# Kernel optimization log

Measured on AMD Instinct MI355X. Metric: run time of the kernel, lower is better.

## Reference

```python
import jax, jax.numpy as jnp
import numpy as np

V, E, H, L = 10000, 256, 512, 2
B, T, S = 64, 64, 128
NEG = -1e6


def setup_inputs() -> dict:
    key = jax.random.key(0)
    ks = jax.random.split(key, 20)
    sc = 0.02
    inp = {
        "x": jax.random.randint(ks[0], (B, T), 0, V),
        "enc_outputs": jax.random.normal(ks[1], (B, S, H), jnp.float32),
        "h0": jax.random.normal(ks[2], (L, B, H), jnp.float32),
        "valid_lens": jax.random.randint(ks[3], (B,), 1, S + 1).astype(jnp.int32),
        # params
        "emb": jax.random.normal(ks[4], (V, E), jnp.float32) * sc,
        "Wq": jax.random.normal(ks[5], (H, H), jnp.float32) * sc,
        "Wk": jax.random.normal(ks[6], (H, H), jnp.float32) * sc,
        "wv": jax.random.normal(ks[7], (H,), jnp.float32) * sc,
        "W_ih0": jax.random.normal(ks[8], (3 * H, H + E), jnp.float32) * sc,
        "W_hh0": jax.random.normal(ks[9], (3 * H, H), jnp.float32) * sc,
        "b_ih0": jnp.zeros((3 * H,), jnp.float32),
        "b_hh0": jnp.zeros((3 * H,), jnp.float32),
        "W_ih1": jax.random.normal(ks[10], (3 * H, H), jnp.float32) * sc,
        "W_hh1": jax.random.normal(ks[11], (3 * H, H), jnp.float32) * sc,
        "b_ih1": jnp.zeros((3 * H,), jnp.float32),
        "b_hh1": jnp.zeros((3 * H,), jnp.float32),
        "Wd": jax.random.normal(ks[12], (V, H), jnp.float32) * sc,
        "bd": jnp.zeros((V,), jnp.float32),
    }
    return inp


def _gru_cell(x, h, W_ih, W_hh, b_ih, b_hh):
    # PyTorch GRU cell math
    gi = x @ W_ih.T + b_ih  # (B, 3H)
    gh = h @ W_hh.T + b_hh
    ir, iz, in_ = jnp.split(gi, 3, axis=-1)
    hr, hz, hn = jnp.split(gh, 3, axis=-1)
    r = jax.nn.sigmoid(ir + hr)
    z = jax.nn.sigmoid(iz + hz)
    n = jnp.tanh(in_ + r * hn)
    return (1.0 - z) * n + z * h


def reference(x, enc_outputs, h0, valid_lens, emb, Wq, Wk, wv,
              W_ih0, W_hh0, b_ih0, b_hh0, W_ih1, W_hh1, b_ih1, b_hh1, Wd, bd):
    X = emb[x]                     # (B, T, E)
    Xt = jnp.transpose(X, (1, 0, 2))  # (T, B, E) time-major
    k_proj = jnp.einsum('bsh,oh->bso', enc_outputs, Wk)  # precompute W_k(keys)
    mask = jnp.arange(S)[None, :] < valid_lens[:, None]  # (B, S)

    def step(h, x_t):
        q = h[-1]                                      # (B, H) last-layer hidden
        q_proj = q @ Wq.T                              # (B, H)
        feats = jnp.tanh(q_proj[:, None, :] + k_proj)  # (B, S, H)
        scores = jnp.einsum('bsh,h->bs', feats, wv)
        scores = jnp.where(mask, scores, NEG)
        attn = jax.nn.softmax(scores, axis=-1)
        context = jnp.einsum('bs,bsh->bh', attn, enc_outputs)
        inp = jnp.concatenate([context, x_t], axis=-1)  # (B, H+E)
        h0n = _gru_cell(inp, h[0], W_ih0, W_hh0, b_ih0, b_hh0)
        h1n = _gru_cell(h0n, h[1], W_ih1, W_hh1, b_ih1, b_hh1)
        hn = jnp.stack([h0n, h1n])
        return hn, h1n

    _, ys = jax.lax.scan(step, h0, Xt)       # ys: (T, B, H)
    logits = jnp.einsum('tbh,vh->tbv', ys, Wd) + bd
    return jnp.transpose(logits, (1, 0, 2))  # (B, T, V)
```

## Files before the change

kernel.cpp:

```cpp
#include <hip/hip_runtime.h>
#include <hip/hip_bf16.h>

#define Bd 64
#define Td 64
#define Sd 128
#define Hd 512
#define Ed 256
#define Vd 10000
#define NBLK 256

#define W0IH 0
#define W0HH 4608
#define W1IH 7680
#define W1HH 10752
#define WTOT 13824

typedef __attribute__((ext_vector_type(8))) short bf16x8;
typedef __attribute__((ext_vector_type(4))) float f32x4;

__device__ __forceinline__ float fast_tanh(float x) {
  float e = __expf(-2.0f * fabsf(x));
  float r = (1.0f - e) / (1.0f + e);
  return copysignf(r, x);
}
__device__ __forceinline__ float fast_sigmoid(float x) {
  return 1.0f / (1.0f + __expf(-x));
}
__device__ __forceinline__ float bf2f(unsigned short u) {
  return __uint_as_float(((unsigned int)u) << 16);
}
__device__ __forceinline__ void st_llc(float* p, float v) {
  __hip_atomic_store(p, v, __ATOMIC_RELAXED, __HIP_MEMORY_SCOPE_AGENT);
}
__device__ __forceinline__ int q4(int k, int b) {
  return (k >> 2) * 256 + b * 4 + (k & 3);
}

__device__ __forceinline__ void gbar(int* arrive, int* go, int ep, int blk, int tid) {
  __syncthreads();
  if (tid == 0)
    __hip_atomic_store(&arrive[blk], ep, __ATOMIC_RELAXED, __HIP_MEMORY_SCOPE_AGENT);
  if (blk == 0) {
    if (tid < 64) {
      for (;;) {
        int a0 = __hip_atomic_load(&arrive[tid], __ATOMIC_RELAXED,
                                   __HIP_MEMORY_SCOPE_AGENT);
        int a1 = __hip_atomic_load(&arrive[tid + 64], __ATOMIC_RELAXED,
                                   __HIP_MEMORY_SCOPE_AGENT);
        int a2 = __hip_atomic_load(&arrive[tid + 128], __ATOMIC_RELAXED,
                                   __HIP_MEMORY_SCOPE_AGENT);
        int a3 = __hip_atomic_load(&arrive[tid + 192], __ATOMIC_RELAXED,
                                   __HIP_MEMORY_SCOPE_AGENT);
        if (a0 >= ep && a1 >= ep && a2 >= ep && a3 >= ep) break;
        __builtin_amdgcn_s_sleep(2);
      }
    }
    __syncthreads();
    if (tid == 0)
      __hip_atomic_store(go, ep, __ATOMIC_RELAXED, __HIP_MEMORY_SCOPE_AGENT);
  }
  if (tid == 0) {
    while (__hip_atomic_load(go, __ATOMIC_RELAXED, __HIP_MEMORY_SCOPE_AGENT) < ep) {
      __builtin_amdgcn_s_sleep(1);
    }
    __builtin_amdgcn_fence(__ATOMIC_ACQUIRE, "agent");
  }
  __syncthreads();
}

__global__ void k_gemm_kp(const float* __restrict__ A, const float* __restrict__ W,
                          unsigned short* __restrict__ C, int M, int N, int K) {
  __shared__ __align__(16) float As[16][64];
  __shared__ __align__(16) float Ws[16][64];
  int m0 = blockIdx.x * 64, n0 = blockIdx.y * 64;
  int tid = threadIdx.x;
  int tx = tid & 15, ty = tid >> 4;
  float acc[4][4] = {};
  for (int k0 = 0; k0 < K; k0 += 16) {
#pragma unroll
    for (int i = 0; i < 4; i++) {
      int e = tid + i * 256;
      int r = e >> 4, c = e & 15;
      As[c][r] = A[(long)(m0 + r) * K + k0 + c];
      Ws[c][r] = W[(long)(n0 + r) * K + k0 + c];
    }
    __syncthreads();
#pragma unroll
    for (int k = 0; k < 16; k++) {
      float a_[4], w_[4];
#pragma unroll
      for (int i = 0; i < 4; i++) a_[i] = As[k][ty * 4 + i];
#pragma unroll
      for (int j = 0; j < 4; j++) w_[j] = Ws[k][tx * 4 + j];
#pragma unroll
      for (int i = 0; i < 4; i++)
#pragma unroll
        for (int j = 0; j < 4; j++) acc[i][j] += a_[i] * w_[j];
    }
    __syncthreads();
  }
#pragma unroll
  for (int i = 0; i < 4; i++)
#pragma unroll
    for (int j = 0; j < 4; j++) {
      __hip_bfloat16 h = __float2bfloat16(acc[i][j]);
      C[(long)(m0 + ty * 4 + i) * N + n0 + tx * 4 + j] = *(unsigned short*)&h;
    }
}

__global__ __launch_bounds__(256) void k_logits(
    const unsigned short* __restrict__ ysbf, const unsigned short* __restrict__ Wdbf,
    const float* __restrict__ bd, float* __restrict__ out, int N) {
  int m0 = blockIdx.x * 64, n0 = blockIdx.y * 64;
  int w = threadIdx.x >> 6, lane = threadIdx.x & 63;
  int row = lane & 15, kg = lane >> 4;
  int mw = m0 + w * 16;
  f32x4 acc[4] = {};
  const unsigned short* Arow = ysbf + (size_t)(mw + row) * 512 + kg * 8;
  for (int k0 = 0; k0 < 512; k0 += 32) {
    bf16x8 af = *(const bf16x8*)(Arow + k0);
#pragma unroll
    for (int nn = 0; nn < 4; nn++) {
      int ncol = n0 + nn * 16 + row;
      bf16x8 bfv = {};
      if (ncol < N) bfv = *(const bf16x8*)(Wdbf + (size_t)ncol * 512 + k0 + kg * 8);
      acc[nn] = __builtin_amdgcn_mfma_f32_16x16x32_bf16(af, bfv, acc[nn], 0, 0, 0);
    }
  }
#pragma unroll
  for (int nn = 0; nn < 4; nn++) {
    int ncol = n0 + nn * 16 + row;
    if (ncol < N) {
      float bv = bd[ncol];
#pragma unroll
      for (int r = 0; r < 4; r++) {
        int mm = mw + kg * 4 + r;
        int t_ = mm >> 6, b_ = mm & 63;
        out[((size_t)(b_ * Td + t_)) * N + ncol] = acc[nn][r] + bv;
      }
    }
  }
}

__global__ void k_tobf(const float* __restrict__ src, unsigned short* __restrict__ dst,
                       long n) {
  long i = (long)blockIdx.x * 1024 + threadIdx.x;
  if (i < n) {
    __hip_bfloat16 h = __float2bfloat16(src[i]);
    dst[i] = *(unsigned short*)&h;
  }
}

__global__ void k_embT(const int* __restrict__ x, const float* __restrict__ emb,
                       float* __restrict__ embTf) {
  __shared__ int rows[64];
  int t = blockIdx.x;
  if (threadIdx.x < 64) rows[threadIdx.x] = x[threadIdx.x * Td + t];
  __syncthreads();
  int e = threadIdx.x;
  for (int b = 0; b < 64; b++) {
    embTf[(size_t)t * 16384 + q4(e, b)] = emb[(long)rows[b] * Ed + e];
  }
}

template <bool C0>
__device__ __forceinline__ void cell_phase(
    int blk, int tid, int t, const float* __restrict__ aT,
    const float* __restrict__ embTf, const float* __restrict__ hT,
    const float* wIH, const float* wHH, const float* __restrict__ bih,
    const float* __restrict__ bhh, const float* __restrict__ den,
    float* __restrict__ houtT, unsigned short* __restrict__ ysbf, float* scratch) {
  int lane = tid & 63;
  int w = tid >> 6;
  const int RIH = C0 ? 768 : 512;
  float* ps = scratch;
  float* psE = scratch + 3072;
  if (w < 8) {
    int strm = w >> 2, qk = w & 3;
    const float* A = (strm == 0 ? aT : hT) + qk * 32 * 256;
    float a[6] = {0.f, 0.f, 0.f, 0.f, 0.f, 0.f};
#pragma unroll 8
    for (int k4 = 0; k4 < 32; k4++) {
      float4 av = *(const float4*)&A[k4 * 256 + lane * 4];
#pragma unroll
      for (int r = 0; r < 6; r++) {
        const float* wr = (strm == 0 ? wIH + (size_t)r * RIH : wHH + (size_t)r * 512) +
                          qk * 128 + k4 * 4;
        float4 w4 = *(const float4*)wr;
        a[r] += av.x * w4.x + av.y * w4.y + av.z * w4.z + av.w * w4.w;
      }
    }
    int base = strm * 6;
#pragma unroll
    for (int r = 0; r < 6; r++) ps[((base + r) * 4 + qk) * 64 + lane] = a[r];
  } else if (C0 && w < 12) {
    int qe = w - 8;
    const float* ef = embTf + (size_t)t * 16384 + qe * 16 * 256;
    float a[6] = {0.f, 0.f, 0.f, 0.f, 0.f, 0.f};
#pragma unroll 8
    for (int k4 = 0; k4 < 16; k4++) {
      float4 ev = *(const float4*)&ef[k4 * 256 + lane * 4];
#pragma unroll
      for (int r = 0; r < 6; r++) {
        const float* wr = wIH + (size_t)r * 768 + 512 + qe * 64 + k4 * 4;
        float4 w4 = *(const float4*)wr;
        a[r] += ev.x * w4.x + ev.y * w4.y + ev.z * w4.z + ev.w * w4.w;
      }
    }
#pragma unroll
    for (int r = 0; r < 6; r++) psE[(r * 4 + qe) * 64 + lane] = a[r];
  }
  __syncthreads();
  if (tid < 128) {
    int jl = tid >> 6, b = tid & 63;
    float invd = C0 ? (1.0f / den[b]) : 1.0f;
#define RD(R)                                                              \
  (ps[((R)*4 + 0) * 64 + b] + ps[((R)*4 + 1) * 64 + b] +                   \
   ps[((R)*4 + 2) * 64 + b] + ps[((R)*4 + 3) * 64 + b])
#define RE(R)                                                              \
  (psE[((R)*4 + 0) * 64 + b] + psE[((R)*4 + 1) * 64 + b] +                 \
   psE[((R)*4 + 2) * 64 + b] + psE[((R)*4 + 3) * 64 + b])
    float ir = RD(0 + jl);
    float iz = RD(2 + jl);
    float in = RD(4 + jl);
    if (C0) {
      ir = ir * invd + RE(0 + jl);
      iz = iz * invd + RE(2 + jl);
      in = in * invd + RE(4 + jl);
    }
    float hr = RD(6 + jl);
    float hz = RD(8 + jl);
    float hn_ = RD(10 + jl);
#undef RD
#undef RE
    int j = blk * 2 + jl;
    float r = fast_sigmoid(ir + hr + bih[j] + bhh[j]);
    float z = fast_sigmoid(iz + hz + bih[Hd + j] + bhh[Hd + j]);
    float n = fast_tanh(in + bih[2 * Hd + j] + r * (hn_ + bhh[2 * Hd + j]));
    float hp = hT[q4(j, b)];
    float out = (1.f - z) * n + z * hp;
    st_llc(&houtT[q4(j, b)], out);
    if (!C0) {
      __hip_bfloat16 hb = __float2bfloat16(out);
      ysbf[((size_t)t * 64 + b) * 512 + j] = *(unsigned short*)&hb;
    }
  }
}

__global__ __launch_bounds__(1024, 1) void k_decoder(
    const float* __restrict__ h0_in, const int* __restrict__ vlen,
    const float* __restrict__ Wq, const float* __restrict__ wvp,
    const float* __restrict__ Wih0, const float* __restrict__ Whh0,
    const float* __restrict__ bih0, const float* __restrict__ bhh0,
    const float* __restrict__ Wih1, const float* __restrict__ Whh1,
    const float* __restrict__ bih1, const float* __restrict__ bhh1,
    const unsigned short* __restrict__ kpbf, const unsigned short* __restrict__ encbf,
    const float* __restrict__ embTf, int* bar, float* qpN, float* ctxT,
    float* den, float* h0TA, float* h0TB, float* h1TA, float* h1TB,
    unsigned short* ysbf) {
  __shared__ __align__(16) float wLDS[WTOT];
  __shared__ __align__(16) float WqL[1024];
  __shared__ __align__(16) unsigned short kpL[32 * 512];
  __shared__ __align__(16) unsigned short encL[32 * 512];
  __shared__ __align__(16) float scratch[4608];
  int blk = blockIdx.x, tid = threadIdx.x;
  int lane = tid & 63;
  int w = tid >> 6;
  int battn = blk >> 2, q = blk & 3;
  int* arrive = bar;
  int* go = bar + NBLK;
  int ep = 0;

  {
    int j0 = blk * 2;
#pragma unroll
    for (int rr = 0; rr < 6; rr++) {
      int g = rr >> 1, jl = rr & 1;
      int row = g * Hd + j0 + jl;
      const float* s0 = Wih0 + (size_t)row * 768;
      for (int k = tid; k < 768; k += 1024) wLDS[W0IH + rr * 768 + k] = s0[k];
      const float* s1 = Whh0 + (size_t)row * Hd;
      for (int k = tid; k < Hd; k += 1024) wLDS[W0HH + rr * 512 + k] = s1[k];
      const float* s2 = Wih1 + (size_t)row * Hd;
      for (int k = tid; k < Hd; k += 1024) wLDS[W1IH + rr * 512 + k] = s2[k];
      const float* s3 = Whh1 + (size_t)row * Hd;
      for (int k = tid; k < Hd; k += 1024) wLDS[W1HH + rr * 512 + k] = s3[k];
    }
    WqL[tid] = Wq[(size_t)(blk * 2 + (tid >> 9)) * Hd + (tid & 511)];
    const uint4* ksrc = (const uint4*)(kpbf + ((size_t)battn * Sd + q * 32) * Hd);
    const uint4* esrc = (const uint4*)(encbf + ((size_t)battn * Sd + q * 32) * Hd);
    uint4* kdst = (uint4*)kpL;
    uint4* edst = (uint4*)encL;
    for (int i = tid; i < 2048; i += 1024) {
      kdst[i] = ksrc[i];
      edst[i] = esrc[i];
    }
  }
  float wvr[8];
#pragma unroll
  for (int i = 0; i < 8; i++) wvr[i] = wvp[lane * 8 + i];

  if (blk < Bd) {
    int b = blk;
    for (int k = tid; k < Hd; k += 1024) {
      st_llc(&h0TA[q4(k, b)], h0_in[(0 * Bd + b) * Hd + k]);
      st_llc(&h1TA[q4(k, b)], h0_in[(1 * Bd + b) * Hd + k]);
    }
  }
  if (tid < 128) st_llc(&ctxT[blk * 128 + tid], 0.f);
  if (blk < Bd && tid == 128) st_llc(&den[blk], 0.f);
  gbar(arrive, go, ++ep, blk, tid);

  for (int t = 0; t < Td; t++) {
    const float* h0prev = (t & 1) ? h0TB : h0TA;
    float* h0next = (t & 1) ? h0TA : h0TB;
    const float* h1prev = (t & 1) ? h1TB : h1TA;
    float* h1next = (t & 1) ? h1TA : h1TB;

    {
      int rl = w >> 3, ks = w & 7;
      const float* qrow = &WqL[rl * 512 + ks * 64];
      const float* hp4 = h1prev + (ks * 16) * 256 + lane * 4;
      float acc = 0.f;
#pragma unroll
      for (int kk = 0; kk < 64; kk += 4) {
        float4 hv = *(const float4*)&hp4[(kk >> 2) * 256];
        acc += hv.x * qrow[kk] + hv.y * qrow[kk + 1] + hv.z * qrow[kk + 2] +
               hv.w * qrow[kk + 3];
      }
      scratch[w * 64 + lane] = acc;
      __syncthreads();
      if (tid < 128) {
        int rl2 = tid >> 6, b = tid & 63;
        float s = 0.f;
#pragma unroll
        for (int qq = 0; qq < 8; qq++) s += scratch[(rl2 * 8 + qq) * 64 + b];
        st_llc(&qpN[(size_t)b * 512 + blk * 2 + rl2], s);
      }
    }
    gbar(arrive, go, ++ep, blk, tid);

    {
      int b = battn;
      float* sc = scratch;
      float qv[8];
      const float* qb = qpN + (size_t)b * 512 + lane * 8;
#pragma unroll
      for (int i = 0; i < 8; i++) qv[i] = qb[i];
      int vl = vlen[b];
#pragma unroll
      for (int si = 0; si < 2; si++) {
        int sl = w * 2 + si;
        uint4 kw = *(const uint4*)&kpL[sl * 512 + lane * 8];
        float f0 = __uint_as_float(kw.x << 16);
        float f1 = __uint_as_float(kw.x & 0xffff0000u);
        float f2 = __uint_as_float(kw.y << 16);
        float f3 = __uint_as_float(kw.y & 0xffff0000u);
        float f4 = __uint_as_float(kw.z << 16);
        float f5 = __uint_as_float(kw.z & 0xffff0000u);
        float f6 = __uint_as_float(kw.w << 16);
        float f7 = __uint_as_float(kw.w & 0xffff0000u);
        float acc = wvr[0] * fast_tanh(qv[0] + f0) + wvr[1] * fast_tanh(qv[1] + f1) +
                    wvr[2] * fast_tanh(qv[2] + f2) + wvr[3] * fast_tanh(qv[3] + f3) +
                    wvr[4] * fast_tanh(qv[4] + f4) + wvr[5] * fast_tanh(qv[5] + f5) +
                    wvr[6] * fast_tanh(qv[6] + f6) + wvr[7] * fast_tanh(qv[7] + f7);
#pragma unroll
        for (int off = 1; off < 64; off <<= 1) acc += __shfl_xor(acc, off);
        if (lane == 0) {
          int s = q * 32 + sl;
          sc[sl] = (s < vl) ? __expf(acc) : 0.f;
        }
      }
      __syncthreads();
      if (tid < 32) {
        float p2 = sc[tid];
#pragma unroll
        for (int off = 1; off < 32; off <<= 1) p2 += __shfl_xor(p2, off, 32);
        if (tid == 0) atomicAdd(&den[b], p2);
      }
      if (tid < 512) {
        float acc = 0.f;
#pragma unroll 8
        for (int s = 0; s < 32; s++) acc += sc[s] * bf2f(encL[s * 512 + tid]);
        atomicAdd(&ctxT[q4(tid, b)], acc);
      }
    }
    gbar(arrive, go, ++ep, blk, tid);

    cell_phase<true>(blk, tid, t, ctxT, embTf, h0prev, wLDS + W0IH, wLDS + W0HH,
                     bih0, bhh0, den, h0next, nullptr, scratch);
    gbar(arrive, go, ++ep, blk, tid);

    if (tid < 128) st_llc(&ctxT[blk * 128 + tid], 0.f);
    if (blk < Bd && tid == 128) st_llc(&den[blk], 0.f);
    cell_phase<false>(blk, tid, t, h0next, nullptr, h1prev, wLDS + W1IH,
                      wLDS + W1HH, bih1, bhh1, nullptr, h1next, ysbf, scratch);
    gbar(arrive, go, ++ep, blk, tid);
  }
}

extern "C" void kernel_launch(void* const* d_in, const int* in_sizes, int n_in,
                              void* d_out, int out_size, void* d_ws, size_t ws_size,
                              hipStream_t stream) {
  const int* x = (const int*)d_in[0];
  const float* enc = (const float*)d_in[1];
  const float* h0 = (const float*)d_in[2];
  const int* vlen = (const int*)d_in[3];
  const float* emb = (const float*)d_in[4];
  const float* Wq = (const float*)d_in[5];
  const float* Wk = (const float*)d_in[6];
  const float* wv = (const float*)d_in[7];
  const float* W_ih0 = (const float*)d_in[8];
  const float* W_hh0 = (const float*)d_in[9];
  const float* b_ih0 = (const float*)d_in[10];
  const float* b_hh0 = (const float*)d_in[11];
  const float* W_ih1 = (const float*)d_in[12];
  const float* W_hh1 = (const float*)d_in[13];
  const float* b_ih1 = (const float*)d_in[14];
  const float* b_hh1 = (const float*)d_in[15];
  const float* Wd = (const float*)d_in[16];
  const float* bd = (const float*)d_in[17];
  float* out = (float*)d_out;

  char* p = (char*)d_ws;
  int* bar = (int*)p;
  p += 2048;
  unsigned short* kpbf = (unsigned short*)p;
  p += (size_t)Bd * Sd * Hd * 2;
  unsigned short* encbf = (unsigned short*)p;
  p += (size_t)Bd * Sd * Hd * 2;
  unsigned short* Wdbf = (unsigned short*)p;
  p += (size_t)Vd * Hd * 2;
  unsigned short* ysbf = (unsigned short*)p;
  p += (size_t)Td * Bd * Hd * 2;
  float* embTf = (float*)p;
  p += (size_t)Td * Ed * Bd * 4;
  float* qpN = (float*)p;   p += (size_t)Bd * Hd * 4;
  float* ctxT = (float*)p;  p += (size_t)Hd * Bd * 4;
  float* den = (float*)p;   p += 256;
  float* h0TA = (float*)p;  p += (size_t)Hd * Bd * 4;
  float* h0TB = (float*)p;  p += (size_t)Hd * Bd * 4;
  float* h1TA = (float*)p;  p += (size_t)Hd * Bd * 4;
  float* h1TB = (float*)p;

  hipMemsetAsync(bar, 0, 2048, stream);

  k_gemm_kp<<<dim3(128, 8), 256, 0, stream>>>(enc, Wk, kpbf, Bd * Sd, Hd, Hd);
  long nenc = (long)Bd * Sd * Hd;
  k_tobf<<<(nenc + 1023) / 1024, 1024, 0, stream>>>(enc, encbf, nenc);
  long nwd = (long)Vd * Hd;
  k_tobf<<<(nwd + 1023) / 1024, 1024, 0, stream>>>(Wd, Wdbf, nwd);
  k_embT<<<Td, 256, 0, stream>>>(x, emb, embTf);
  k_decoder<<<NBLK, 1024, 0, stream>>>(h0, vlen, Wq, wv, W_ih0, W_hh0, b_ih0,
                                       b_hh0, W_ih1, W_hh1, b_ih1, b_hh1, kpbf,
                                       encbf, embTf, bar, qpN, ctxT, den, h0TA,
                                       h0TB, h1TA, h1TB, ysbf);
  k_logits<<<dim3(64, 157), 256, 0, stream>>>(ysbf, Wdbf, bd, out, Vd);
}
```

Before: 3.762 ms.

## Precompute embedding input-gate projections for all timesteps outside the recurrent loop

```diff
diff --git a/kernel.cpp b/kernel.cpp
--- a/kernel.cpp
+++ b/kernel.cpp
@@ -108,6 +108,47 @@
     }
 }
 
+__global__ void k_embG(const int* __restrict__ x, const float* __restrict__ emb,
+                       const float* __restrict__ Wih0, float* __restrict__ embG) {
+  __shared__ __align__(16) float As[16][64];
+  __shared__ __align__(16) float Bs[16][64];
+  __shared__ int xs[64];
+  int m0 = blockIdx.x * 64, t = blockIdx.y;
+  int tid = threadIdx.x;
+  int tx = tid & 15, ty = tid >> 4;
+  if (tid < 64) xs[tid] = x[tid * Td + t];
+  __syncthreads();
+  float acc[4][4] = {};
+  for (int k0 = 0; k0 < Ed; k0 += 16) {
+#pragma unroll
+    for (int i = 0; i < 4; i++) {
+      int e = tid + i * 256;
+      int r = e >> 4, c = e & 15;
+      As[c][r] = Wih0[(size_t)(m0 + r) * 768 + 512 + k0 + c];
+      Bs[c][r] = emb[(size_t)xs[r] * Ed + k0 + c];
+    }
+    __syncthreads();
+#pragma unroll
+    for (int k = 0; k < 16; k++) {
+      float a_[4], b_[4];
+#pragma unroll
+      for (int i = 0; i < 4; i++) a_[i] = As[k][ty * 4 + i];
+#pragma unroll
+      for (int j = 0; j < 4; j++) b_[j] = Bs[k][tx * 4 + j];
+#pragma unroll
+      for (int i = 0; i < 4; i++)
+#pragma unroll
+        for (int j = 0; j < 4; j++) acc[i][j] += a_[i] * b_[j];
+    }
+    __syncthreads();
+  }
+#pragma unroll
+  for (int i = 0; i < 4; i++)
+#pragma unroll
+    for (int j = 0; j < 4; j++)
+      embG[(size_t)(m0 + ty * 4 + i) * 4096 + t * 64 + tx * 4 + j] = acc[i][j];
+}
+
 __global__ __launch_bounds__(256) void k_logits(
     const unsigned short* __restrict__ ysbf, const unsigned short* __restrict__ Wdbf,
     const float* __restrict__ bd, float* __restrict__ out, int N) {
@@ -151,22 +192,10 @@
   }
 }
 
-__global__ void k_embT(const int* __restrict__ x, const float* __restrict__ emb,
-                       float* __restrict__ embTf) {
-  __shared__ int rows[64];
-  int t = blockIdx.x;
-  if (threadIdx.x < 64) rows[threadIdx.x] = x[threadIdx.x * Td + t];
-  __syncthreads();
-  int e = threadIdx.x;
-  for (int b = 0; b < 64; b++) {
-    embTf[(size_t)t * 16384 + q4(e, b)] = emb[(long)rows[b] * Ed + e];
-  }
-}
-
 template <bool C0>
 __device__ __forceinline__ void cell_phase(
     int blk, int tid, int t, const float* __restrict__ aT,
-    const float* __restrict__ embTf, const float* __restrict__ hT,
+    const float* __restrict__ embG, const float* __restrict__ hT,
     const float* wIH, const float* wHH, const float* __restrict__ bih,
     const float* __restrict__ bhh, const float* __restrict__ den,
     float* __restrict__ houtT, unsigned short* __restrict__ ysbf, float* scratch) {
@@ -174,66 +203,52 @@
   int w = tid >> 6;
   const int RIH = C0 ? 768 : 512;
   float* ps = scratch;
-  float* psE = scratch + 3072;
-  if (w < 8) {
-    int strm = w >> 2, qk = w & 3;
-    const float* A = (strm == 0 ? aT : hT) + qk * 32 * 256;
+  {
+    int strm = w >> 3, e8 = w & 7;
+    const float* A = (strm == 0 ? aT : hT) + e8 * 16 * 256;
     float a[6] = {0.f, 0.f, 0.f, 0.f, 0.f, 0.f};
-#pragma unroll 8
-    for (int k4 = 0; k4 < 32; k4++) {
+#pragma unroll
+    for (int k4 = 0; k4 < 16; k4++) {
       float4 av = *(const float4*)&A[k4 * 256 + lane * 4];
 #pragma unroll
       for (int r = 0; r < 6; r++) {
         const float* wr = (strm == 0 ? wIH + (size_t)r * RIH : wHH + (size_t)r * 512) +
-                          qk * 128 + k4 * 4;
+                          e8 * 64 + k4 * 4;
         float4 w4 = *(const float4*)wr;
         a[r] += av.x * w4.x + av.y * w4.y + av.z * w4.z + av.w * w4.w;
       }
     }
+    if (C0 && strm == 0) {
+      float inv = 1.0f / den[lane];
+#pragma unroll
+      for (int r = 0; r < 6; r++) a[r] *= inv;
+    }
     int base = strm * 6;
 #pragma unroll
-    for (int r = 0; r < 6; r++) ps[((base + r) * 4 + qk) * 64 + lane] = a[r];
-  } else if (C0 && w < 12) {
-    int qe = w - 8;
-    const float* ef = embTf + (size_t)t * 16384 + qe * 16 * 256;
-    float a[6] = {0.f, 0.f, 0.f, 0.f, 0.f, 0.f};
-#pragma unroll 8
-    for (int k4 = 0; k4 < 16; k4++) {
-      float4 ev = *(const float4*)&ef[k4 * 256 + lane * 4];
-#pragma unroll
-      for (int r = 0; r < 6; r++) {
-        const float* wr = wIH + (size_t)r * 768 + 512 + qe * 64 + k4 * 4;
-        float4 w4 = *(const float4*)wr;
-        a[r] += ev.x * w4.x + ev.y * w4.y + ev.z * w4.z + ev.w * w4.w;
-      }
-    }
-#pragma unroll
-    for (int r = 0; r < 6; r++) psE[(r * 4 + qe) * 64 + lane] = a[r];
+    for (int r = 0; r < 6; r++) ps[((base + r) * 8 + e8) * 64 + lane] = a[r];
   }
   __syncthreads();
   if (tid < 128) {
     int jl = tid >> 6, b = tid & 63;
-    float invd = C0 ? (1.0f / den[b]) : 1.0f;
-#define RD(R)                                                              \
-  (ps[((R)*4 + 0) * 64 + b] + ps[((R)*4 + 1) * 64 + b] +                   \
-   ps[((R)*4 + 2) * 64 + b] + ps[((R)*4 + 3) * 64 + b])
-#define RE(R)                                                              \
-  (psE[((R)*4 + 0) * 64 + b] + psE[((R)*4 + 1) * 64 + b] +                 \
-   psE[((R)*4 + 2) * 64 + b] + psE[((R)*4 + 3) * 64 + b])
+    int j = blk * 2 + jl;
+#define RD(R)                                                                   \
+  (ps[((R)*8 + 0) * 64 + b] + ps[((R)*8 + 1) * 64 + b] +                        \
+   ps[((R)*8 + 2) * 64 + b] + ps[((R)*8 + 3) * 64 + b] +                        \
+   ps[((R)*8 + 4) * 64 + b] + ps[((R)*8 + 5) * 64 + b] +                        \
+   ps[((R)*8 + 6) * 64 + b] + ps[((R)*8 + 7) * 64 + b])
     float ir = RD(0 + jl);
     float iz = RD(2 + jl);
     float in = RD(4 + jl);
     if (C0) {
-      ir = ir * invd + RE(0 + jl);
-      iz = iz * invd + RE(2 + jl);
-      in = in * invd + RE(4 + jl);
+      int col = t * 64 + b;
+      ir += embG[(size_t)j * 4096 + col];
+      iz += embG[(size_t)(512 + j) * 4096 + col];
+      in += embG[(size_t)(1024 + j) * 4096 + col];
     }
     float hr = RD(6 + jl);
     float hz = RD(8 + jl);
     float hn_ = RD(10 + jl);
 #undef RD
-#undef RE
-    int j = blk * 2 + jl;
     float r = fast_sigmoid(ir + hr + bih[j] + bhh[j]);
     float z = fast_sigmoid(iz + hz + bih[Hd + j] + bhh[Hd + j]);
     float n = fast_tanh(in + bih[2 * Hd + j] + r * (hn_ + bhh[2 * Hd + j]));
@@ -255,14 +270,14 @@
     const float* __restrict__ Wih1, const float* __restrict__ Whh1,
     const float* __restrict__ bih1, const float* __restrict__ bhh1,
     const unsigned short* __restrict__ kpbf, const unsigned short* __restrict__ encbf,
-    const float* __restrict__ embTf, int* bar, float* qpN, float* ctxT,
+    const float* __restrict__ embG, int* bar, float* qpN, float* ctxT,
     float* den, float* h0TA, float* h0TB, float* h1TA, float* h1TB,
     unsigned short* ysbf) {
   __shared__ __align__(16) float wLDS[WTOT];
   __shared__ __align__(16) float WqL[1024];
   __shared__ __align__(16) unsigned short kpL[32 * 512];
   __shared__ __align__(16) unsigned short encL[32 * 512];
-  __shared__ __align__(16) float scratch[4608];
+  __shared__ __align__(16) float scratch[6144];
   int blk = blockIdx.x, tid = threadIdx.x;
   int lane = tid & 63;
   int w = tid >> 6;
@@ -387,7 +402,7 @@
     }
     gbar(arrive, go, ++ep, blk, tid);
 
-    cell_phase<true>(blk, tid, t, ctxT, embTf, h0prev, wLDS + W0IH, wLDS + W0HH,
+    cell_phase<true>(blk, tid, t, ctxT, embG, h0prev, wLDS + W0IH, wLDS + W0HH,
                      bih0, bhh0, den, h0next, nullptr, scratch);
     gbar(arrive, go, ++ep, blk, tid);
 
@@ -433,8 +448,8 @@
   p += (size_t)Vd * Hd * 2;
   unsigned short* ysbf = (unsigned short*)p;
   p += (size_t)Td * Bd * Hd * 2;
-  float* embTf = (float*)p;
-  p += (size_t)Td * Ed * Bd * 4;
+  float* embG = (float*)p;
+  p += (size_t)1536 * 4096 * 4;
   float* qpN = (float*)p;   p += (size_t)Bd * Hd * 4;
   float* ctxT = (float*)p;  p += (size_t)Hd * Bd * 4;
   float* den = (float*)p;   p += 256;
@@ -450,10 +465,10 @@
   k_tobf<<<(nenc + 1023) / 1024, 1024, 0, stream>>>(enc, encbf, nenc);
   long nwd = (long)Vd * Hd;
   k_tobf<<<(nwd + 1023) / 1024, 1024, 0, stream>>>(Wd, Wdbf, nwd);
-  k_embT<<<Td, 256, 0, stream>>>(x, emb, embTf);
+  k_embG<<<dim3(24, Td), 256, 0, stream>>>(x, emb, W_ih0, embG);
   k_decoder<<<NBLK, 1024, 0, stream>>>(h0, vlen, Wq, wv, W_ih0, W_hh0, b_ih0,
                                        b_hh0, W_ih1, W_hh1, b_ih1, b_hh1, kpbf,
-                                       encbf, embTf, bar, qpN, ctxT, den, h0TA,
+                                       encbf, embG, bar, qpN, ctxT, den, h0TA,
                                        h0TB, h1TA, h1TB, ysbf);
   k_logits<<<dim3(64, 157), 256, 0, stream>>>(ysbf, Wdbf, bd, out, Vd);
 }
```

Result: slower. 3.914 ms (+4.1%).
